# Optimization experiments

Hardware: AMD Instinct MI355X
Metric: run time of the kernel (lower is better)

Reference implementation:

```python
import jax, jax.numpy as jnp
import numpy as np

J = 1.0
B, C, L = 16, 16, 128


def _masks(L):
    ii, jj = jnp.meshgrid(jnp.arange(L), jnp.arange(L), indexing='ij')
    black = ((ii + jj) % 2 == 0)
    return black, jnp.logical_not(black)


def _nbr_sum(s):
    # periodic up/down/left/right neighbor sum, same math as the (i±1)%L gathers
    return (jnp.roll(s, 1, -2) + jnp.roll(s, -1, -2)
            + jnp.roll(s, 1, -1) + jnp.roll(s, -1, -1))


def _half_update(spins, mask, T, key):
    # Metropolis on one checkerboard color: dE = 2*J*s*sum_nbrs
    dE = 2.0 * J * spins * _nbr_sum(spins)
    u = jax.random.uniform(key, spins.shape, dtype=spins.dtype)
    accept = u < jnp.exp(-dE / T[:, None, None, None])
    return jnp.where(jnp.logical_and(accept, mask), -spins, spins)


def _one_sweep(spins, T, key, black, white):
    k1, k2 = jax.random.split(key)
    spins = _half_update(spins, black, T, k1)
    return _half_update(spins, white, T, k2)


def _energy(spins):
    # E = -J * sum over bonds (right + down neighbors once each) -> [B, C]
    return -J * jnp.sum(spins * (jnp.roll(spins, -1, -2) + jnp.roll(spins, -1, -1)), axis=(-2, -1))


def _pt_exchange(spins, T, key):
    nB = T.shape[0]
    P = nB // 2
    E = _energy(spins)                       # [B, C]
    beta = 1.0 / T
    E0, E1 = E[0:2 * P:2], E[1:2 * P:2]
    d = (beta[0:2 * P:2] - beta[1:2 * P:2])[:, None] * (E0 - E1)  # [P, C]
    u = jax.random.uniform(key, d.shape, dtype=spins.dtype)
    # accept prob min(1, exp(d)); exp(min(d,0)) is overflow-safe and equivalent
    acc = (u < jnp.exp(jnp.minimum(d, 0.0)))[:, :, None, None]
    s0, s1 = spins[0:2 * P:2], spins[1:2 * P:2]
    spins = spins.at[0:2 * P:2].set(jnp.where(acc, s1, s0))
    spins = spins.at[1:2 * P:2].set(jnp.where(acc, s0, s1))
    return spins


def _simulate(spins_init, T, n_sweeps, n_therm, decorrelate, pt_interval):
    Lx = spins_init.shape[-1]
    black, white = _masks(Lx)
    base = jax.random.key(42)

    def step_fn(spins, i):
        k = jax.random.fold_in(base, i)
        spins = _one_sweep(spins, T, k, black, white)
        spins = jax.lax.cond(i % pt_interval == 0,
                             lambda s: _pt_exchange(s, T, jax.random.fold_in(k, 123)),
                             lambda s: s, spins)
        return spins, None

    # thermalization
    spins, _ = jax.lax.scan(step_fn, spins_init, jnp.arange(n_therm))

    # production: record one sample per decorrelate sweeps
    num_samples = n_sweeps // decorrelate

    def block_fn(spins, b):
        spins, _ = jax.lax.scan(lambda s, j: step_fn(s, n_therm + b * decorrelate + j),
                                spins, jnp.arange(decorrelate))
        return spins, spins

    spins, samples = jax.lax.scan(block_fn, spins, jnp.arange(num_samples))
    # samples: [S, B, C, L, L] -> [B, C*S, L, L]
    Bn, Cn = spins.shape[0], spins.shape[1]
    return jnp.transpose(samples, (1, 0, 2, 3, 4)).reshape(Bn, num_samples * Cn, Lx, Lx)


def setup_inputs() -> dict:
    key = jax.random.key(0)
    k1, _ = jax.random.split(key)
    x = jax.random.normal(k1, (B, C, L, L), dtype=jnp.float32)
    spins_init = jnp.where(x >= 0, 1.0, -1.0).astype(jnp.float32)  # ±1 Ising spins
    T = jnp.linspace(1.0, 3.5, B).astype(jnp.float32)              # temperature ladder
    return {"spins_init": spins_init, "T": T, "n_sweeps": 10, "n_therm": 10,
            "decorrelate": 5, "pt_interval": 5}


def reference(spins_init, T, n_sweeps, n_therm, decorrelate, pt_interval):
    return _simulate(spins_init, T, n_sweeps, n_therm, decorrelate, pt_interval)
```

## Files before the change

### kernel.cpp

```cpp
#include <hip/hip_runtime.h>
#include <stdint.h>


#define LSZ   128
#define NB    16
#define NC    16
#define NSITES (NB*NC*LSZ*LSZ)

__host__ __device__ __forceinline__ void tf2x32(uint32_t k0, uint32_t k1,
                                                uint32_t x0, uint32_t x1,
                                                uint32_t& o0, uint32_t& o1) {
  uint32_t k2 = k0 ^ k1 ^ 0x1BD11BDAu;
  x0 += k0; x1 += k1;
#define TFR(r) { x0 += x1; x1 = (x1 << (r)) | (x1 >> (32 - (r))); x1 ^= x0; }
  TFR(13) TFR(15) TFR(26) TFR(6)
  x0 += k1; x1 += k2 + 1u;
  TFR(17) TFR(29) TFR(16) TFR(24)
  x0 += k2; x1 += k0 + 2u;
  TFR(13) TFR(15) TFR(26) TFR(6)
  x0 += k0; x1 += k1 + 3u;
  TFR(17) TFR(29) TFR(16) TFR(24)
  x0 += k1; x1 += k2 + 4u;
  TFR(13) TFR(15) TFR(26) TFR(6)
  x0 += k2; x1 += k0 + 5u;
#undef TFR
  o0 = x0; o1 = x1;
}

__device__ __forceinline__ float tf_uniform(uint32_t w) {
  union { uint32_t u; float f; } cvt;
  cvt.u = (w >> 9) | 0x3f800000u;
  return cvt.f - 1.0f;
}

__device__ __forceinline__ int sb(uint32_t w, int b) {
  return (int)((int32_t)(w << ((3 - b) * 8)) >> 24);
}


__global__ __launch_bounds__(256) void k_init(const float4* __restrict__ in,
                                              uint32_t* __restrict__ s4,
                                              int* __restrict__ slotmap,
                                              int* __restrict__ occ) {
  int t = blockIdx.x * 256 + threadIdx.x;
  float4 v = in[t];
  uint32_t o = (v.x >= 0.0f ? 0x01u : 0xFFu)
             | ((v.y >= 0.0f ? 0x01u : 0xFFu) << 8)
             | ((v.z >= 0.0f ? 0x01u : 0xFFu) << 16)
             | ((v.w >= 0.0f ? 0x01u : 0xFFu) << 24);
  s4[t] = o;
  if (t < 256) { slotmap[t] = t >> 4; occ[t] = t; }
}

__global__ __launch_bounds__(1024) void k_chunk(uint32_t* __restrict__ sg,
                                                const float* __restrict__ T,
                                                const int* __restrict__ slotmap,
                                                float* __restrict__ E,
                                                float* __restrict__ out,
                                                uint4 K0, uint4 K1, uint4 K2,
                                                uint4 K3, uint4 K4,
                                                int nsw, int sample_local,
                                                int sidx, int write_E) {
  __shared__ __align__(16) uint32_t lat32[LSZ * LSZ / 4];
  __shared__ int wred[16];

  const int w = blockIdx.x;
  const int t = threadIdx.x;
  const int c = w & 15;
  const int bp = slotmap[w];
  const float Tb = T[bp];
  const float p4 = (float)exp((double)(-4.0f / Tb));
  const float p8 = (float)exp((double)(-8.0f / Tb));

  ((uint4*)lat32)[t] = ((const uint4*)sg)[(w << 10) + t];
  __syncthreads();

  const int r    = t >> 3;
  const int seg  = t & 7;
  const int col0 = seg << 4;
  const uint32_t rowbase = ((uint32_t)((bp << 4) | c) << 14) + ((uint32_t)r << 7);
  const int8_t* latb = (const int8_t*)lat32;

  for (int sw = 0; sw < nsw; ++sw) {
    uint4 kk;
    switch (sw) {
      case 0: kk = K0; break;
      case 1: kk = K1; break;
      case 2: kk = K2; break;
      case 3: kk = K3; break;
      default: kk = K4; break;
    }
    for (int par = 0; par < 2; ++par) {
      const uint32_t kk0 = par ? kk.z : kk.x;
      const uint32_t kk1 = par ? kk.w : kk.y;
      const int j0 = (r + par) & 1;

      uint4 cv = ((const uint4*)lat32)[(r << 3) + seg];
      uint4 uv = ((const uint4*)lat32)[(((r - 1) & 127) << 3) + seg];
      uint4 dv = ((const uint4*)lat32)[(((r + 1) & 127) << 3) + seg];
      int lfb = latb[(r << 7) + ((col0 - 1) & 127)];
      int rtb = latb[(r << 7) + ((col0 + 16) & 127)];

      uint32_t cw[4] = {cv.x, cv.y, cv.z, cv.w};
      uint32_t uw[4] = {uv.x, uv.y, uv.z, uv.w};
      uint32_t dw[4] = {dv.x, dv.y, dv.z, dv.w};

      uint32_t ext[5];
      ext[0] = (cw[0] << 8) | (uint32_t)(uint8_t)lfb;
      ext[1] = (cw[0] >> 24) | (cw[1] << 8);
      ext[2] = (cw[1] >> 24) | (cw[2] << 8);
      ext[3] = (cw[2] >> 24) | (cw[3] << 8);
      ext[4] = (cw[3] >> 24) | ((uint32_t)(uint8_t)rtb << 8);
      uint32_t Y[5], U[4], D[4];
#pragma unroll
      for (int i = 0; i < 4; ++i) {
        uint32_t sh = (ext[i] >> 8) | (ext[i + 1] << 24);
        Y[i] = j0 ? sh : ext[i];
        uint32_t su = (uw[i] >> 8) | ((i < 3 ? uw[i + 1] : 0u) << 24);
        U[i] = j0 ? su : uw[i];
        uint32_t sd = (dw[i] >> 8) | ((i < 3 ? dw[i + 1] : 0u) << 24);
        D[i] = j0 ? sd : dw[i];
      }
      Y[4] = j0 ? (ext[4] >> 8) : ext[4];

      const uint32_t mbase = 0xFEu << (8 * j0);
      uint32_t xm[4] = {0u, 0u, 0u, 0u};
      const uint32_t cnt0 = rowbase + (uint32_t)(col0 + j0);
#pragma unroll
      for (int m = 0; m < 8; ++m) {
        int lf = sb(Y[(2 * m) >> 2], (2 * m) & 3);
        int s0 = sb(Y[(2 * m + 1) >> 2], (2 * m + 1) & 3);
        int rt = sb(Y[(2 * m + 2) >> 2], (2 * m + 2) & 3);
        int up = sb(U[(2 * m) >> 2], (2 * m) & 3);
        int dn = sb(D[(2 * m) >> 2], (2 * m) & 3);
        int q = s0 * (lf + rt + up + dn);
        uint32_t o0, o1;
        tf2x32(kk0, kk1, 0u, cnt0 + 2u * (uint32_t)m, o0, o1);
        float u = tf_uniform(o0 ^ o1);
        bool a = (q <= 0) || (u < (q == 4 ? p8 : p4));
        if (a) xm[m >> 1] |= (m & 1) ? (mbase << 16) : mbase;
      }
      uint4 nv;
      nv.x = cw[0] ^ xm[0]; nv.y = cw[1] ^ xm[1];
      nv.z = cw[2] ^ xm[2]; nv.w = cw[3] ^ xm[3];
      ((uint4*)lat32)[(r << 3) + seg] = nv;
      __syncthreads();
    }

    if (sw == sample_local) {
      uint4 cv = ((const uint4*)lat32)[(r << 3) + seg];
      float4* dst = (float4*)out
                  + (((size_t)((bp << 5) + (sidx << 4) + c)) << 12)
                  + (r << 5) + (seg << 2);
      uint32_t wv[4] = {cv.x, cv.y, cv.z, cv.w};
#pragma unroll
      for (int q = 0; q < 4; ++q) {
        float4 f;
        f.x = (float)sb(wv[q], 0); f.y = (float)sb(wv[q], 1);
        f.z = (float)sb(wv[q], 2); f.w = (float)sb(wv[q], 3);
        dst[q] = f;
      }
    }
  }

  ((uint4*)sg)[(w << 10) + t] = ((const uint4*)lat32)[t];

  if (write_E) {
    uint4 cv = ((const uint4*)lat32)[(r << 3) + seg];
    uint4 dv = ((const uint4*)lat32)[(((r + 1) & 127) << 3) + seg];
    int rb = latb[(r << 7) + ((col0 + 16) & 127)];
    uint32_t cw[4] = {cv.x, cv.y, cv.z, cv.w};
    uint32_t dw[4] = {dv.x, dv.y, dv.z, dv.w};
    int psum = 0;
#pragma unroll
    for (int i = 0; i < 16; ++i) {
      int ci = sb(cw[i >> 2], i & 3);
      int di = sb(dw[i >> 2], i & 3);
      int ri = (i < 15) ? sb(cw[(i + 1) >> 2], (i + 1) & 3) : rb;
      psum += ci * (di + ri);
    }
#pragma unroll
    for (int o = 32; o > 0; o >>= 1) psum += __shfl_down(psum, o, 64);
    if ((t & 63) == 0) wred[t >> 6] = psum;
    __syncthreads();
    if (t == 0) {
      int tot = 0;
#pragma unroll
      for (int i = 0; i < 16; ++i) tot += wred[i];
      E[(bp << 4) | c] = -(float)tot;
    }
  }
}

__global__ __launch_bounds__(128) void k_decide(const float* __restrict__ E,
                                                const float* __restrict__ T,
                                                uint32_t pk0, uint32_t pk1,
                                                int* __restrict__ slotmap,
                                                int* __restrict__ occ) {
  int t = threadIdx.x;
  int p = t >> 4, c = t & 15;
  float E0 = E[(2 * p) * NC + c];
  float E1 = E[(2 * p + 1) * NC + c];
  float b0 = 1.0f / T[2 * p];
  float b1 = 1.0f / T[2 * p + 1];
  float d = (b0 - b1) * (E0 - E1);
  uint32_t w0, w1;
  tf2x32(pk0, pk1, 0u, (uint32_t)t, w0, w1);
  float u = tf_uniform(w0 ^ w1);
  float pa = (d < 0.0f) ? (float)exp((double)d) : 1.0f;
  if (u < pa) {
    int a = occ[(2 * p) * NC + c];
    int b = occ[(2 * p + 1) * NC + c];
    occ[(2 * p) * NC + c] = b;
    occ[(2 * p + 1) * NC + c] = a;
    slotmap[a] = 2 * p + 1;
    slotmap[b] = 2 * p;
  }
}

extern "C" void kernel_launch(void* const* d_in, const int* in_sizes, int n_in,
                              void* d_out, int out_size, void* d_ws, size_t ws_size,
                              hipStream_t stream) {
  const float* spins_in = (const float*)d_in[0];
  const float* T        = (const float*)d_in[1];
  uint32_t* s   = (uint32_t*)d_ws;
  float*  E     = (float*)((char*)d_ws + (4u << 20));
  int*  slotmap = (int*)((char*)d_ws + (4u << 20) + 1024);
  int*  occ     = (int*)((char*)d_ws + (4u << 20) + 2048);
  float*  out = (float*)d_out;

  k_init<<<NSITES / 4 / 256, 256, 0, stream>>>((const float4*)spins_in, s,
                                               slotmap, occ);

  const uint32_t bk0 = 0u, bk1 = 42u;
  const int starts[5]  = {0, 1, 6, 11, 16};
  const int counts[5]  = {1, 5, 5, 5, 4};
  const int samploc[5] = {-1, -1, -1, 3, 3};
  const int sampidx[5] = {0, 0, 0, 0, 1};
  const int writeE[5]  = {1, 1, 1, 1, 0};

  for (int ch = 0; ch < 5; ++ch) {
    uint4 K[5] = {{0,0,0,0},{0,0,0,0},{0,0,0,0},{0,0,0,0},{0,0,0,0}};
    for (int sw = 0; sw < counts[ch]; ++sw) {
      int i = starts[ch] + sw;
      uint32_t kk0, kk1, k1a, k1b, k2a, k2b;
      tf2x32(bk0, bk1, 0u, (uint32_t)i, kk0, kk1);
      tf2x32(kk0, kk1, 0u, 0u, k1a, k1b);
      tf2x32(kk0, kk1, 0u, 1u, k2a, k2b);
      K[sw].x = k1a; K[sw].y = k1b; K[sw].z = k2a; K[sw].w = k2b;
    }
    k_chunk<<<256, 1024, 0, stream>>>(s, T, slotmap, E, out,
                                      K[0], K[1], K[2], K[3], K[4],
                                      counts[ch], samploc[ch], sampidx[ch],
                                      writeE[ch]);
    if (writeE[ch]) {
      int i = starts[ch] + counts[ch] - 1;
      uint32_t kk0, kk1, p0, p1;
      tf2x32(bk0, bk1, 0u, (uint32_t)i, kk0, kk1);
      tf2x32(kk0, kk1, 0u, 123u, p0, p1);
      k_decide<<<1, 128, 0, stream>>>(E, T, p0, p1, slotmap, occ);
    }
  }
}
```

Measured before the change: 292.0 us.

## Fuse init and replica-exchange decision into chunk kernel, halve block threads

The separate init kernel and per-chunk exchange-decision kernel are removed. Spin packing now happens inside the first chunk kernel, and each block makes its own parallel-tempering swap decision from the previous chunk's energies, using ping-pong energy buffers. Blocks drop from 1024 to 512 threads, with each thread updating 32 sites instead of 16. RNG keys are computed on the device, and the last chunk skips writing the lattice back. The goal is fewer launches and less global traffic, at the cost of more per-thread register pressure and serial work on thread 0.

```diff
diff --git a/kernel.cpp b/kernel.cpp
--- a/kernel.cpp
+++ b/kernel.cpp
@@ -37,97 +37,133 @@
   return (int)((int32_t)(w << ((3 - b) * 8)) >> 24);
 }
 
-
-__global__ __launch_bounds__(256) void k_init(const float4* __restrict__ in,
-                                              uint32_t* __restrict__ s4,
-                                              int* __restrict__ slotmap,
-                                              int* __restrict__ occ) {
-  int t = blockIdx.x * 256 + threadIdx.x;
-  float4 v = in[t];
-  uint32_t o = (v.x >= 0.0f ? 0x01u : 0xFFu)
-             | ((v.y >= 0.0f ? 0x01u : 0xFFu) << 8)
-             | ((v.z >= 0.0f ? 0x01u : 0xFFu) << 16)
-             | ((v.w >= 0.0f ? 0x01u : 0xFFu) << 24);
-  s4[t] = o;
-  if (t < 256) { slotmap[t] = t >> 4; occ[t] = t; }
-}
-
-__global__ __launch_bounds__(1024) void k_chunk(uint32_t* __restrict__ sg,
-                                                const float* __restrict__ T,
-                                                const int* __restrict__ slotmap,
-                                                float* __restrict__ E,
-                                                float* __restrict__ out,
-                                                uint4 K0, uint4 K1, uint4 K2,
-                                                uint4 K3, uint4 K4,
-                                                int nsw, int sample_local,
-                                                int sidx, int write_E) {
+__global__ __launch_bounds__(512) void k_chunk(const float4* __restrict__ in4,
+                                               uint32_t* __restrict__ sg,
+                                               const float* __restrict__ T,
+                                               int* __restrict__ slotmap,
+                                               const float* __restrict__ Eprev,
+                                               float* __restrict__ Ecur,
+                                               float* __restrict__ out,
+                                               int chunk, int start, int nsw,
+                                               int sample_local, int sidx,
+                                               int write_E, int store_back) {
   __shared__ __align__(16) uint32_t lat32[LSZ * LSZ / 4];
-  __shared__ int wred[16];
+  __shared__ uint32_t kb[5][4];
+  __shared__ float sh_p4, sh_p8;
+  __shared__ int sh_bp;
+  __shared__ int wred[8];
 
   const int w = blockIdx.x;
   const int t = threadIdx.x;
   const int c = w & 15;
-  const int bp = slotmap[w];
-  const float Tb = T[bp];
-  const float p4 = (float)exp((double)(-4.0f / Tb));
-  const float p8 = (float)exp((double)(-8.0f / Tb));
-
-  ((uint4*)lat32)[t] = ((const uint4*)sg)[(w << 10) + t];
+
+  if (t < nsw) {
+    uint32_t kk0, kk1, a, b;
+    tf2x32(0u, 42u, 0u, (uint32_t)(start + t), kk0, kk1);
+    tf2x32(kk0, kk1, 0u, 0u, a, b);
+    kb[t][0] = a; kb[t][1] = b;
+    tf2x32(kk0, kk1, 0u, 1u, a, b);
+    kb[t][2] = a; kb[t][3] = b;
+  }
+
+  if (chunk == 0) {
+    for (int k = 0; k < 8; ++k) {
+      int idx = k * 512 + t;
+      float4 v = in4[(w << 12) + idx];
+      lat32[idx] = (v.x >= 0.0f ? 0x01u : 0xFFu)
+                 | ((v.y >= 0.0f ? 0x01u : 0xFFu) << 8)
+                 | ((v.z >= 0.0f ? 0x01u : 0xFFu) << 16)
+                 | ((v.w >= 0.0f ? 0x01u : 0xFFu) << 24);
+    }
+  } else {
+    for (int k = 0; k < 2; ++k)
+      ((uint4*)lat32)[k * 512 + t] = ((const uint4*)sg)[(w << 10) + k * 512 + t];
+  }
+
+  if (t == 0) {
+    int bp;
+    if (chunk == 0) {
+      bp = w >> 4;
+    } else {
+      bp = slotmap[w];
+      int p = bp >> 1;
+      float E0 = Eprev[(2 * p) * NC + c];
+      float E1 = Eprev[(2 * p + 1) * NC + c];
+      float b0 = 1.0f / T[2 * p];
+      float b1 = 1.0f / T[2 * p + 1];
+      float d = (b0 - b1) * (E0 - E1);
+      uint32_t kk0, kk1, p0, p1, w0, w1;
+      tf2x32(0u, 42u, 0u, (uint32_t)(start - 1), kk0, kk1);
+      tf2x32(kk0, kk1, 0u, 123u, p0, p1);
+      tf2x32(p0, p1, 0u, (uint32_t)(p * NC + c), w0, w1);
+      float u = tf_uniform(w0 ^ w1);
+      float pa = (d < 0.0f) ? (float)exp((double)d) : 1.0f;
+      if (u < pa) bp ^= 1;
+    }
+    slotmap[w] = bp;
+    sh_bp = bp;
+    float Tb = T[bp];
+    sh_p4 = (float)exp((double)(-4.0f / Tb));
+    sh_p8 = (float)exp((double)(-8.0f / Tb));
+  }
   __syncthreads();
 
-  const int r    = t >> 3;
-  const int seg  = t & 7;
-  const int col0 = seg << 4;
+  const int bp = sh_bp;
+  const float p4 = sh_p4, p8 = sh_p8;
+  const int r    = t >> 2;
+  const int sg32 = t & 3;
+  const int col0 = sg32 << 5;
   const uint32_t rowbase = ((uint32_t)((bp << 4) | c) << 14) + ((uint32_t)r << 7);
   const int8_t* latb = (const int8_t*)lat32;
+  const int own4 = (r << 3) + (sg32 << 1);
 
   for (int sw = 0; sw < nsw; ++sw) {
-    uint4 kk;
-    switch (sw) {
-      case 0: kk = K0; break;
-      case 1: kk = K1; break;
-      case 2: kk = K2; break;
-      case 3: kk = K3; break;
-      default: kk = K4; break;
-    }
     for (int par = 0; par < 2; ++par) {
-      const uint32_t kk0 = par ? kk.z : kk.x;
-      const uint32_t kk1 = par ? kk.w : kk.y;
+      const uint32_t kk0 = kb[sw][par * 2];
+      const uint32_t kk1 = kb[sw][par * 2 + 1];
       const int j0 = (r + par) & 1;
 
-      uint4 cv = ((const uint4*)lat32)[(r << 3) + seg];
-      uint4 uv = ((const uint4*)lat32)[(((r - 1) & 127) << 3) + seg];
-      uint4 dv = ((const uint4*)lat32)[(((r + 1) & 127) << 3) + seg];
+      uint32_t cw[8], uw[8], dw[8];
+      {
+        uint4 a  = ((const uint4*)lat32)[own4];
+        uint4 b2 = ((const uint4*)lat32)[own4 + 1];
+        cw[0]=a.x; cw[1]=a.y; cw[2]=a.z; cw[3]=a.w;
+        cw[4]=b2.x; cw[5]=b2.y; cw[6]=b2.z; cw[7]=b2.w;
+        int u4 = (((r - 1) & 127) << 3) + (sg32 << 1);
+        a  = ((const uint4*)lat32)[u4];
+        b2 = ((const uint4*)lat32)[u4 + 1];
+        uw[0]=a.x; uw[1]=a.y; uw[2]=a.z; uw[3]=a.w;
+        uw[4]=b2.x; uw[5]=b2.y; uw[6]=b2.z; uw[7]=b2.w;
+        int d4 = (((r + 1) & 127) << 3) + (sg32 << 1);
+        a  = ((const uint4*)lat32)[d4];
+        b2 = ((const uint4*)lat32)[d4 + 1];
+        dw[0]=a.x; dw[1]=a.y; dw[2]=a.z; dw[3]=a.w;
+        dw[4]=b2.x; dw[5]=b2.y; dw[6]=b2.z; dw[7]=b2.w;
+      }
       int lfb = latb[(r << 7) + ((col0 - 1) & 127)];
-      int rtb = latb[(r << 7) + ((col0 + 16) & 127)];
-
-      uint32_t cw[4] = {cv.x, cv.y, cv.z, cv.w};
-      uint32_t uw[4] = {uv.x, uv.y, uv.z, uv.w};
-      uint32_t dw[4] = {dv.x, dv.y, dv.z, dv.w};
-
-      uint32_t ext[5];
-      ext[0] = (cw[0] << 8) | (uint32_t)(uint8_t)lfb;
-      ext[1] = (cw[0] >> 24) | (cw[1] << 8);
-      ext[2] = (cw[1] >> 24) | (cw[2] << 8);
-      ext[3] = (cw[2] >> 24) | (cw[3] << 8);
-      ext[4] = (cw[3] >> 24) | ((uint32_t)(uint8_t)rtb << 8);
-      uint32_t Y[5], U[4], D[4];
-#pragma unroll
-      for (int i = 0; i < 4; ++i) {
-        uint32_t sh = (ext[i] >> 8) | (ext[i + 1] << 24);
-        Y[i] = j0 ? sh : ext[i];
-        uint32_t su = (uw[i] >> 8) | ((i < 3 ? uw[i + 1] : 0u) << 24);
-        U[i] = j0 ? su : uw[i];
-        uint32_t sd = (dw[i] >> 8) | ((i < 3 ? dw[i + 1] : 0u) << 24);
-        D[i] = j0 ? sd : dw[i];
-      }
-      Y[4] = j0 ? (ext[4] >> 8) : ext[4];
+      int rtb = latb[(r << 7) + ((col0 + 32) & 127)];
+
+      uint32_t ex[9];
+      ex[0] = (cw[0] << 8) | (uint32_t)(uint8_t)lfb;
+#pragma unroll
+      for (int i = 1; i < 8; ++i) ex[i] = (cw[i - 1] >> 24) | (cw[i] << 8);
+      ex[8] = (cw[7] >> 24) | ((uint32_t)(uint8_t)rtb << 8);
+      uint32_t Y[9], U[8], D[8];
+#pragma unroll
+      for (int i = 0; i < 8; ++i) {
+        Y[i] = j0 ? ((ex[i] >> 8) | (ex[i + 1] << 24)) : ex[i];
+        U[i] = j0 ? ((uw[i] >> 8) | ((i < 7 ? uw[i + 1] : 0u) << 24)) : uw[i];
+        D[i] = j0 ? ((dw[i] >> 8) | ((i < 7 ? dw[i + 1] : 0u) << 24)) : dw[i];
+      }
+      Y[8] = j0 ? (ex[8] >> 8) : ex[8];
 
       const uint32_t mbase = 0xFEu << (8 * j0);
-      uint32_t xm[4] = {0u, 0u, 0u, 0u};
+      uint32_t xm[8];
+#pragma unroll
+      for (int i = 0; i < 8; ++i) xm[i] = 0u;
       const uint32_t cnt0 = rowbase + (uint32_t)(col0 + j0);
 #pragma unroll
-      for (int m = 0; m < 8; ++m) {
+      for (int m = 0; m < 16; ++m) {
         int lf = sb(Y[(2 * m) >> 2], (2 * m) & 3);
         int s0 = sb(Y[(2 * m + 1) >> 2], (2 * m + 1) & 3);
         int rt = sb(Y[(2 * m + 2) >> 2], (2 * m + 2) & 3);
@@ -140,43 +176,52 @@
         bool a = (q <= 0) || (u < (q == 4 ? p8 : p4));
         if (a) xm[m >> 1] |= (m & 1) ? (mbase << 16) : mbase;
       }
-      uint4 nv;
-      nv.x = cw[0] ^ xm[0]; nv.y = cw[1] ^ xm[1];
-      nv.z = cw[2] ^ xm[2]; nv.w = cw[3] ^ xm[3];
-      ((uint4*)lat32)[(r << 3) + seg] = nv;
+      uint4 n0, n1;
+      n0.x = cw[0] ^ xm[0]; n0.y = cw[1] ^ xm[1];
+      n0.z = cw[2] ^ xm[2]; n0.w = cw[3] ^ xm[3];
+      n1.x = cw[4] ^ xm[4]; n1.y = cw[5] ^ xm[5];
+      n1.z = cw[6] ^ xm[6]; n1.w = cw[7] ^ xm[7];
+      ((uint4*)lat32)[own4]     = n0;
+      ((uint4*)lat32)[own4 + 1] = n1;
       __syncthreads();
     }
 
     if (sw == sample_local) {
-      uint4 cv = ((const uint4*)lat32)[(r << 3) + seg];
       float4* dst = (float4*)out
                   + (((size_t)((bp << 5) + (sidx << 4) + c)) << 12)
-                  + (r << 5) + (seg << 2);
-      uint32_t wv[4] = {cv.x, cv.y, cv.z, cv.w};
-#pragma unroll
-      for (int q = 0; q < 4; ++q) {
+                  + (r << 5) + (sg32 << 3);
+      const uint32_t* own = lat32 + (r << 5) + (sg32 << 3);
+#pragma unroll
+      for (int qd = 0; qd < 8; ++qd) {
+        uint32_t v = own[qd];
         float4 f;
-        f.x = (float)sb(wv[q], 0); f.y = (float)sb(wv[q], 1);
-        f.z = (float)sb(wv[q], 2); f.w = (float)sb(wv[q], 3);
-        dst[q] = f;
-      }
-    }
-  }
-
-  ((uint4*)sg)[(w << 10) + t] = ((const uint4*)lat32)[t];
+        f.x = (float)sb(v, 0); f.y = (float)sb(v, 1);
+        f.z = (float)sb(v, 2); f.w = (float)sb(v, 3);
+        dst[qd] = f;
+      }
+    }
+  }
 
   if (write_E) {
-    uint4 cv = ((const uint4*)lat32)[(r << 3) + seg];
-    uint4 dv = ((const uint4*)lat32)[(((r + 1) & 127) << 3) + seg];
-    int rb = latb[(r << 7) + ((col0 + 16) & 127)];
-    uint32_t cw[4] = {cv.x, cv.y, cv.z, cv.w};
-    uint32_t dw[4] = {dv.x, dv.y, dv.z, dv.w};
+    uint32_t cw[8], dw[8];
+    {
+      uint4 a  = ((const uint4*)lat32)[own4];
+      uint4 b2 = ((const uint4*)lat32)[own4 + 1];
+      cw[0]=a.x; cw[1]=a.y; cw[2]=a.z; cw[3]=a.w;
+      cw[4]=b2.x; cw[5]=b2.y; cw[6]=b2.z; cw[7]=b2.w;
+      int d4 = (((r + 1) & 127) << 3) + (sg32 << 1);
+      a  = ((const uint4*)lat32)[d4];
+      b2 = ((const uint4*)lat32)[d4 + 1];
+      dw[0]=a.x; dw[1]=a.y; dw[2]=a.z; dw[3]=a.w;
+      dw[4]=b2.x; dw[5]=b2.y; dw[6]=b2.z; dw[7]=b2.w;
+    }
+    int rb = latb[(r << 7) + ((col0 + 32) & 127)];
     int psum = 0;
 #pragma unroll
-    for (int i = 0; i < 16; ++i) {
+    for (int i = 0; i < 32; ++i) {
       int ci = sb(cw[i >> 2], i & 3);
       int di = sb(dw[i >> 2], i & 3);
-      int ri = (i < 15) ? sb(cw[(i + 1) >> 2], (i + 1) & 3) : rb;
+      int ri = (i < 31) ? sb(cw[(i + 1) >> 2], (i + 1) & 3) : rb;
       psum += ci * (di + ri);
     }
 #pragma unroll
@@ -186,35 +231,14 @@
     if (t == 0) {
       int tot = 0;
 #pragma unroll
-      for (int i = 0; i < 16; ++i) tot += wred[i];
-      E[(bp << 4) | c] = -(float)tot;
-    }
-  }
-}
-
-__global__ __launch_bounds__(128) void k_decide(const float* __restrict__ E,
-                                                const float* __restrict__ T,
-                                                uint32_t pk0, uint32_t pk1,
-                                                int* __restrict__ slotmap,
-                                                int* __restrict__ occ) {
-  int t = threadIdx.x;
-  int p = t >> 4, c = t & 15;
-  float E0 = E[(2 * p) * NC + c];
-  float E1 = E[(2 * p + 1) * NC + c];
-  float b0 = 1.0f / T[2 * p];
-  float b1 = 1.0f / T[2 * p + 1];
-  float d = (b0 - b1) * (E0 - E1);
-  uint32_t w0, w1;
-  tf2x32(pk0, pk1, 0u, (uint32_t)t, w0, w1);
-  float u = tf_uniform(w0 ^ w1);
-  float pa = (d < 0.0f) ? (float)exp((double)d) : 1.0f;
-  if (u < pa) {
-    int a = occ[(2 * p) * NC + c];
-    int b = occ[(2 * p + 1) * NC + c];
-    occ[(2 * p) * NC + c] = b;
-    occ[(2 * p + 1) * NC + c] = a;
-    slotmap[a] = 2 * p + 1;
-    slotmap[b] = 2 * p;
+      for (int i = 0; i < 8; ++i) tot += wred[i];
+      Ecur[(bp << 4) | c] = -(float)tot;
+    }
+  }
+
+  if (store_back) {
+    for (int k = 0; k < 2; ++k)
+      ((uint4*)sg)[(w << 10) + k * 512 + t] = ((const uint4*)lat32)[k * 512 + t];
   }
 }
 
@@ -224,41 +248,25 @@
   const float* spins_in = (const float*)d_in[0];
   const float* T        = (const float*)d_in[1];
   uint32_t* s   = (uint32_t*)d_ws;
-  float*  E     = (float*)((char*)d_ws + (4u << 20));
-  int*  slotmap = (int*)((char*)d_ws + (4u << 20) + 1024);
-  int*  occ     = (int*)((char*)d_ws + (4u << 20) + 2048);
+  float*  Ea    = (float*)((char*)d_ws + (4u << 20));
+  float*  Eb    = (float*)((char*)d_ws + (4u << 20) + 1024);
+  int*  slotmap = (int*)((char*)d_ws + (4u << 20) + 2048);
   float*  out = (float*)d_out;
 
-  k_init<<<NSITES / 4 / 256, 256, 0, stream>>>((const float4*)spins_in, s,
-                                               slotmap, occ);
-
-  const uint32_t bk0 = 0u, bk1 = 42u;
   const int starts[5]  = {0, 1, 6, 11, 16};
   const int counts[5]  = {1, 5, 5, 5, 4};
   const int samploc[5] = {-1, -1, -1, 3, 3};
   const int sampidx[5] = {0, 0, 0, 0, 1};
   const int writeE[5]  = {1, 1, 1, 1, 0};
+  const int storeB[5]  = {1, 1, 1, 1, 0};
 
   for (int ch = 0; ch < 5; ++ch) {
-    uint4 K[5] = {{0,0,0,0},{0,0,0,0},{0,0,0,0},{0,0,0,0},{0,0,0,0}};
-    for (int sw = 0; sw < counts[ch]; ++sw) {
-      int i = starts[ch] + sw;
-      uint32_t kk0, kk1, k1a, k1b, k2a, k2b;
-      tf2x32(bk0, bk1, 0u, (uint32_t)i, kk0, kk1);
-      tf2x32(kk0, kk1, 0u, 0u, k1a, k1b);
-      tf2x32(kk0, kk1, 0u, 1u, k2a, k2b);
-      K[sw].x = k1a; K[sw].y = k1b; K[sw].z = k2a; K[sw].w = k2b;
-    }
-    k_chunk<<<256, 1024, 0, stream>>>(s, T, slotmap, E, out,
-                                      K[0], K[1], K[2], K[3], K[4],
-                                      counts[ch], samploc[ch], sampidx[ch],
-                                      writeE[ch]);
-    if (writeE[ch]) {
-      int i = starts[ch] + counts[ch] - 1;
-      uint32_t kk0, kk1, p0, p1;
-      tf2x32(bk0, bk1, 0u, (uint32_t)i, kk0, kk1);
-      tf2x32(kk0, kk1, 0u, 123u, p0, p1);
-      k_decide<<<1, 128, 0, stream>>>(E, T, p0, p1, slotmap, occ);
-    }
-  }
-}
+    float* Ecur  = (ch & 1) ? Eb : Ea;
+    float* Eprev = (ch & 1) ? Ea : Eb;
+    k_chunk<<<256, 512, 0, stream>>>((const float4*)spins_in, s, T, slotmap,
+                                     Eprev, Ecur, out,
+                                     ch, starts[ch], counts[ch],
+                                     samploc[ch], sampidx[ch],
+                                     writeE[ch], storeB[ch]);
+  }
+}
```

Result: no change. 290.6 us (-0.5%).
